# Performance work log

Hardware: AMD Instinct MI355X
Metric: run time of the kernel (lower is better)

Reference implementation:

```python
import jax, jax.numpy as jnp
import numpy as np
import math

B, N, D = 4, 2048, 512
H, DH = 8, 128
INNER = H * DH


def setup_inputs() -> dict:
    key = jax.random.key(0)
    k1, k2, k3, k4 = jax.random.split(key, 4)
    x = jax.random.normal(k1, (B, N, D), dtype=jnp.float32)
    Wg = jax.random.normal(k2, (D, INNER), dtype=jnp.float32) * (1.0 / math.sqrt(D))
    Wout = jax.random.normal(k3, (INNER, D), dtype=jnp.float32) * (1.0 / math.sqrt(INNER))
    sigma = jax.random.uniform(k4, (1, H, 1, 1), dtype=jnp.float32, minval=0.5, maxval=2.5)
    return {"x": x, "Wg": Wg, "Wout": Wout, "sigma": sigma}


def reference(x, Wg, Wout, sigma):
    b, n, d = x.shape
    h, dh = H, DH
    # value projection: [b,n,d] @ [d, h*dh] -> [b,h,n,dh]
    v = (x @ Wg).reshape(b, n, h, dh).transpose(0, 2, 1, 3)
    # fixed Gaussian positional mask, shared across batch: build once per head
    pos = jnp.arange(1, n + 1, dtype=jnp.float32)
    diffs = jnp.abs(pos[:, None] - pos[None, :])  # [n, n]
    sig = sigma.reshape(h, 1, 1)  # [h,1,1]
    inv_norm = 1.0 / (jnp.sqrt(2.0 * jnp.float32(math.pi)) * sig)
    gauss = inv_norm * jnp.exp(-(diffs[None] ** 2) / (2.0 * sig ** 2))  # [h,n,n]
    corr = gauss / gauss.sum(-1, keepdims=True)  # row-normalized [h,n,n]
    # attention: broadcast mask over batch
    attn = jnp.einsum('hnm,bhmd->bhnd', corr, v)
    out = attn.transpose(0, 2, 1, 3).reshape(b, n, h * dh)
    return out @ Wout  # dropout p=0.0 -> identity
```

## Files before the change

kernel.cpp:

```cpp
#include <hip/hip_runtime.h>
#include <hip/hip_bf16.h>
#include <math.h>

#define B_ 4
#define N_ 2048
#define D_ 512
#define H_ 8
#define DH_ 128
#define INNER_ 1024
#define W_ 32
#define M_ (B_ * N_)

typedef __attribute__((ext_vector_type(8))) short short8;
typedef __attribute__((ext_vector_type(4))) float floatx4;

typedef const __attribute__((address_space(1))) char* gcp;
typedef __attribute__((address_space(3))) char* lcp;

__device__ __forceinline__ float bf16hi_to_f(unsigned u) {
    union { unsigned u; float f; } c; c.u = u; return c.f;
}

template <typename OutT>
__global__ __launch_bounds__(256, 4) void gemm_bf16_dbuf(
    const __hip_bfloat16* __restrict__ A, const __hip_bfloat16* __restrict__ Bt,
    OutT* __restrict__ C, int M, int N, int K)
{
    __shared__ char smem[32768];

    const int tid  = threadIdx.x;
    const int lane = tid & 63;
    const int w    = tid >> 6;
    const int wm   = w >> 1;
    const int wn   = w & 1;
    const int bm   = blockIdx.y;
    const int bn   = blockIdx.x;

    const int kh = lane >> 4;
    const int ml = lane & 15;

    floatx4 acc[2][2];
    #pragma unroll
    for (int i = 0; i < 2; ++i)
        #pragma unroll
        for (int j = 0; j < 2; ++j) acc[i][j] = (floatx4){0.f, 0.f, 0.f, 0.f};

    const char* Ab = (const char*)(A + (size_t)(bm * 64) * K);
    const char* Bb = (const char*)(Bt + (size_t)(bn * 64) * K);
    const size_t rowstride = (size_t)K * 2;

    auto issue = [&](int buf, int k0) {
        #pragma unroll
        for (int it = 0; it < 2; ++it) {
            int o = it * 4096 + tid * 16;
            int r = o >> 7;
            int s = (o >> 4) & 7;
            int c = s ^ (r & 7);
            size_t goff = (size_t)r * rowstride + (size_t)k0 * 2 + c * 16;
            __builtin_amdgcn_global_load_lds((gcp)(Ab + goff),
                (lcp)(smem + buf * 16384 + o), 16, 0, 0);
            __builtin_amdgcn_global_load_lds((gcp)(Bb + goff),
                (lcp)(smem + buf * 16384 + 8192 + o), 16, 0, 0);
        }
    };

    auto consume = [&](int buf) {
        const short* As = (const short*)(smem + buf * 16384);
        const short* Bs = (const short*)(smem + buf * 16384 + 8192);
        short8 af[2][2], bf[2][2];
        #pragma unroll
        for (int t = 0; t < 2; ++t) {
            int ra = wm * 32 + t * 16 + ml;
            int rb = wn * 32 + t * 16 + ml;
            #pragma unroll
            for (int kk = 0; kk < 2; ++kk) {
                int ch = kk * 4 + kh;
                af[t][kk] = *(const short8*)(As + ra * 64 + ((ch ^ (ra & 7)) * 8));
                bf[t][kk] = *(const short8*)(Bs + rb * 64 + ((ch ^ (rb & 7)) * 8));
            }
        }
        #pragma unroll
        for (int kk = 0; kk < 2; ++kk)
            #pragma unroll
            for (int i = 0; i < 2; ++i)
                #pragma unroll
                for (int j = 0; j < 2; ++j)
                    acc[i][j] = __builtin_amdgcn_mfma_f32_16x16x32_bf16(
                        af[i][kk], bf[j][kk], acc[i][j], 0, 0, 0);
    };

    const int nk = K >> 6;
    issue(0, 0);
    for (int kt = 0; kt < nk; kt += 2) {
        __syncthreads();
        if (kt + 1 < nk) issue(1, (kt + 1) << 6);
        consume(0);
        __syncthreads();
        if (kt + 2 < nk) issue(0, (kt + 2) << 6);
        consume(1);
    }
    __syncthreads();

    float* Cs = (float*)smem;
    const int rq = lane >> 4;
    const int cl = lane & 15;
    #pragma unroll
    for (int i = 0; i < 2; ++i)
        #pragma unroll
        for (int j = 0; j < 2; ++j)
            #pragma unroll
            for (int r = 0; r < 4; ++r)
                Cs[(wm * 32 + i * 16 + rq * 4 + r) * 64 + wn * 32 + j * 16 + cl] = acc[i][j][r];
    __syncthreads();

    if constexpr (sizeof(OutT) == 2) {
        #pragma unroll
        for (int p = 0; p < 2; ++p) {
            int idx = p * 256 + tid;
            int rr = idx >> 3;
            int cc = (idx & 7) * 8;
            const float* src = Cs + rr * 64 + cc;
            __hip_bfloat16 o[8];
            #pragma unroll
            for (int e = 0; e < 8; ++e) o[e] = __float2bfloat16(src[e]);
            *(short8*)((__hip_bfloat16*)C + (size_t)(bm * 64 + rr) * N + bn * 64 + cc) = *(short8*)o;
        }
    } else {
        #pragma unroll
        for (int p = 0; p < 4; ++p) {
            int idx = p * 256 + tid;
            int rr = idx >> 4;
            int cc = (idx & 15) * 4;
            float4 vv = *(const float4*)(Cs + rr * 64 + cc);
            *(float4*)((float*)C + (size_t)(bm * 64 + rr) * N + bn * 64 + cc) = vv;
        }
    }
}

__device__ __forceinline__ void transpose32(
    const float* __restrict__ src, __hip_bfloat16* __restrict__ dst,
    int R, int Cn, int rt, int ct, int tid)
{
    __shared__ float t[32][33];
    int c0 = ct * 32, r0 = rt * 32;
    int lx = tid & 31, ly = tid >> 5;
    #pragma unroll
    for (int i = 0; i < 32; i += 8)
        t[ly + i][lx] = src[(size_t)(r0 + ly + i) * Cn + c0 + lx];
    __syncthreads();
    #pragma unroll
    for (int i = 0; i < 32; i += 8)
        dst[(size_t)(c0 + ly + i) * R + r0 + lx] = __float2bfloat16(t[lx][ly + i]);
}

__global__ __launch_bounds__(256) void prep(
    const float* __restrict__ x, const float* __restrict__ Wg,
    const float* __restrict__ Wout, __hip_bfloat16* __restrict__ x_bf,
    __hip_bfloat16* __restrict__ Wg_t, __hip_bfloat16* __restrict__ Wout_t)
{
    const int bid = blockIdx.x;
    const int tid = threadIdx.x;
    if (bid < 2048) {
        int i = bid * 256 + tid;
        const float4* s = (const float4*)x + (size_t)i * 2;
        float4 a = s[0], b = s[1];
        __hip_bfloat16 o[8] = {
            __float2bfloat16(a.x), __float2bfloat16(a.y), __float2bfloat16(a.z), __float2bfloat16(a.w),
            __float2bfloat16(b.x), __float2bfloat16(b.y), __float2bfloat16(b.z), __float2bfloat16(b.w)};
        *(short8*)(x_bf + (size_t)i * 8) = *(short8*)o;
    } else if (bid < 2560) {
        int id2 = bid - 2048;
        transpose32(Wg, Wg_t, D_, INNER_, id2 >> 5, id2 & 31, tid);
    } else {
        int id2 = bid - 2560;
        transpose32(Wout, Wout_t, INNER_, D_, id2 >> 4, id2 & 15, tid);
    }
}

#define TNA 64
#define ROWSB (TNA + 2 * W_)
#define CHB 64

struct bf16x4s { __hip_bfloat16 a, b, c, d; };

__global__ __launch_bounds__(256) void banded_attn3(
    const __hip_bfloat16* __restrict__ v, const float* __restrict__ sigma,
    __hip_bfloat16* __restrict__ attn)
{
    __shared__ __hip_bfloat16 vs[ROWSB][CHB];
    __shared__ float wtab[2 * W_ + 1];
    __shared__ float winv[TNA];

    const int tid = threadIdx.x;
    const int n0  = blockIdx.x * TNA;
    const int h   = blockIdx.y >> 1;
    const int ch0 = (blockIdx.y & 1) * CHB;
    const int b   = blockIdx.z;

    const __hip_bfloat16* vbase = v + (size_t)b * N_ * INNER_ + h * DH_ + ch0;
    #pragma unroll
    for (int it = 0; it < 4; ++it) {
        int idx = tid + it * 256;
        int r = idx >> 3;
        int g = idx & 7;
        int m = n0 - W_ + r;
        int4 val = make_int4(0, 0, 0, 0);
        if (m >= 0 && m < N_) val = *(const int4*)(vbase + (size_t)m * INNER_ + g * 8);
        *(int4*)&vs[r][g * 8] = val;
    }
    if (tid <= 2 * W_) {
        float sig = sigma[h];
        float d = (float)(tid - W_);
        wtab[tid] = __expf(-d * d / (2.0f * sig * sig));
    }
    __syncthreads();

    if (tid < TNA) {
        int n = n0 + tid;
        float ws = 0.f;
        #pragma unroll
        for (int j = 0; j <= 2 * W_; ++j) {
            int m = n - W_ + j;
            ws += (m >= 0 && m < N_) ? wtab[j] : 0.f;
        }
        winv[tid] = 1.0f / ws;
    }
    __syncthreads();

    const int cg = tid & 15;
    const int rg = tid >> 4;

    float4 acc[4];
    #pragma unroll
    for (int r = 0; r < 4; ++r) acc[r] = make_float4(0.f, 0.f, 0.f, 0.f);
    float wreg[4] = {0.f, 0.f, 0.f, 0.f};

    const unsigned* vrow0 = (const unsigned*)&vs[rg * 4][cg * 4];

    #pragma unroll 4
    for (int l = 0; l < 2 * W_ + 4; ++l) {
        wreg[l & 3] = (l <= 2 * W_) ? wtab[l] : 0.f;
        const unsigned* p = vrow0 + (size_t)l * (CHB / 2);
        unsigned r0 = p[0], r1 = p[1];
        float4 vv;
        vv.x = bf16hi_to_f(r0 << 16);
        vv.y = bf16hi_to_f(r0 & 0xffff0000u);
        vv.z = bf16hi_to_f(r1 << 16);
        vv.w = bf16hi_to_f(r1 & 0xffff0000u);
        #pragma unroll
        for (int r = 0; r < 4; ++r) {
            float wgt = wreg[(l - r) & 3];
            acc[r].x += wgt * vv.x; acc[r].y += wgt * vv.y;
            acc[r].z += wgt * vv.z; acc[r].w += wgt * vv.w;
        }
    }

    #pragma unroll
    for (int r = 0; r < 4; ++r) {
        int nl = rg * 4 + r;
        float s = winv[nl];
        bf16x4s o = { __float2bfloat16(acc[r].x * s), __float2bfloat16(acc[r].y * s),
                      __float2bfloat16(acc[r].z * s), __float2bfloat16(acc[r].w * s) };
        *(bf16x4s*)(attn + ((size_t)b * N_ + n0 + nl) * INNER_ + h * DH_ + ch0 + cg * 4) = o;
    }
}

extern "C" void kernel_launch(void* const* d_in, const int* in_sizes, int n_in,
                              void* d_out, int out_size, void* d_ws, size_t ws_size,
                              hipStream_t stream) {
    const float* x     = (const float*)d_in[0];
    const float* Wg    = (const float*)d_in[1];
    const float* Wout  = (const float*)d_in[2];
    const float* sigma = (const float*)d_in[3];
    float* out = (float*)d_out;

    char* ws = (char*)d_ws;
    __hip_bfloat16* x_bf   = (__hip_bfloat16*)ws;
    __hip_bfloat16* Wg_t   = (__hip_bfloat16*)(ws + (((size_t)8)  << 20));
    __hip_bfloat16* Wout_t = (__hip_bfloat16*)(ws + (((size_t)9)  << 20));
    __hip_bfloat16* v_bf   = (__hip_bfloat16*)(ws + (((size_t)10) << 20));
    __hip_bfloat16* attn   = (__hip_bfloat16*)(ws + (((size_t)26) << 20));

    prep<<<dim3(3072), dim3(256), 0, stream>>>(x, Wg, Wout, x_bf, Wg_t, Wout_t);

    gemm_bf16_dbuf<__hip_bfloat16><<<dim3(INNER_ / 64, M_ / 64), dim3(256), 0, stream>>>(
        x_bf, Wg_t, v_bf, M_, INNER_, D_);

    banded_attn3<<<dim3(N_ / TNA, H_ * 2, B_), dim3(256), 0, stream>>>(v_bf, sigma, attn);

    gemm_bf16_dbuf<float><<<dim3(D_ / 64, M_ / 64), dim3(256), 0, stream>>>(
        attn, Wout_t, out, M_, D_, INNER_);
}
```

Baseline: 136.2 us.

## Fuse value projection GEMM with banded Gaussian blur in one kernel

Replaces the separate value-projection GEMM and banded attention kernels with one kernel. Each block computes a 128-row slab of v (64 output rows plus a 32-row halo on each side) for one head with MFMA, stages it in LDS as bf16, and then applies the normalized Gaussian band directly. This removes the global write and re-read of the full v tensor and one launch. The cost is recomputing the halo rows, which roughly doubles the projection FLOPs. The K loop is single-buffered. The column permutation that the LDS packing introduces is undone by permuting the K axis of the transposed Wout.

After: 130.2 us. -4.4%, faster.

```diff
diff --git a/kernel.cpp b/kernel.cpp
--- a/kernel.cpp
+++ b/kernel.cpp
@@ -19,6 +19,162 @@
 
 __device__ __forceinline__ float bf16hi_to_f(unsigned u) {
     union { unsigned u; float f; } c; c.u = u; return c.f;
+}
+__device__ __forceinline__ unsigned f_to_bf16bits(float f) {
+    union { float f; unsigned u; } c; c.f = f;
+    return (c.u + 0x7fffu + ((c.u >> 16) & 1u)) >> 16;
+}
+
+struct bf16x4s { __hip_bfloat16 a, b, c, d; };
+
+__global__ __launch_bounds__(256, 4) void g1_blur(
+    const __hip_bfloat16* __restrict__ x_bf,
+    const __hip_bfloat16* __restrict__ Wg_t,
+    const float* __restrict__ sigma,
+    __hip_bfloat16* __restrict__ attn)
+{
+    __shared__ char smem[33824];
+    __hip_bfloat16* Asm = (__hip_bfloat16*)smem;
+    __hip_bfloat16* Bsm = (__hip_bfloat16*)(smem + 16384);
+
+    const int tid  = threadIdx.x;
+    const int lane = tid & 63;
+    const int w    = tid >> 6;
+    const int wm   = w >> 1;
+    const int wn   = w & 1;
+    const int quad = lane >> 4;
+    const int cl   = lane & 15;
+    const int bm   = blockIdx.x;
+    const int h    = blockIdx.y;
+    const int n0   = bm * 64;
+    const int nb0  = n0 & (N_ - 1);
+
+    floatx4 acc[4][4];
+    #pragma unroll
+    for (int i = 0; i < 4; ++i)
+        #pragma unroll
+        for (int j = 0; j < 4; ++j) acc[i][j] = (floatx4){0.f, 0.f, 0.f, 0.f};
+
+    const char* Ab = (const char*)x_bf;
+    const char* Bb = (const char*)(Wg_t + (size_t)(h * DH_) * D_);
+
+    for (int k0 = 0; k0 < D_; k0 += 64) {
+        #pragma unroll
+        for (int it = 0; it < 4; ++it) {
+            int o = it * 4096 + tid * 16;
+            int r = o >> 7;
+            int s = (o >> 4) & 7;
+            int c = s ^ (r & 7);
+            int gr = n0 - W_ + r;
+            gr = gr < 0 ? 0 : (gr > M_ - 1 ? M_ - 1 : gr);
+            __builtin_amdgcn_global_load_lds(
+                (gcp)(Ab + (size_t)gr * 1024 + k0 * 2 + c * 16), (lcp)(smem + o), 16, 0, 0);
+            __builtin_amdgcn_global_load_lds(
+                (gcp)(Bb + (size_t)r * 1024 + k0 * 2 + c * 16), (lcp)(smem + 16384 + o), 16, 0, 0);
+        }
+        __syncthreads();
+
+        const short* As = (const short*)Asm;
+        const short* Bs = (const short*)Bsm;
+        #pragma unroll
+        for (int kk = 0; kk < 2; ++kk) {
+            short8 af[4], bf[4];
+            int ch = kk * 4 + quad;
+            #pragma unroll
+            for (int t = 0; t < 4; ++t) {
+                int ra = wm * 64 + t * 16 + cl;
+                int rb = wn * 64 + t * 16 + cl;
+                af[t] = *(const short8*)(As + ra * 64 + ((ch ^ (ra & 7)) * 8));
+                bf[t] = *(const short8*)(Bs + rb * 64 + ((ch ^ (rb & 7)) * 8));
+            }
+            #pragma unroll
+            for (int i = 0; i < 4; ++i)
+                #pragma unroll
+                for (int j = 0; j < 4; ++j)
+                    acc[i][j] = __builtin_amdgcn_mfma_f32_16x16x32_bf16(
+                        af[i], bf[j], acc[i][j], 0, 0, 0);
+        }
+        __syncthreads();
+    }
+
+    unsigned short* vsp = (unsigned short*)smem;
+    float* wtab = (float*)(smem + 33280);
+    float* winv = (float*)(smem + 33280 + 272);
+
+    #pragma unroll
+    for (int i = 0; i < 4; ++i) {
+        #pragma unroll
+        for (int jp = 0; jp < 2; ++jp) {
+            #pragma unroll
+            for (int rr = 0; rr < 4; ++rr) {
+                int srow = wm * 64 + i * 16 + quad * 4 + rr;
+                int vb = nb0 - W_ + srow;
+                unsigned u = 0u;
+                if (vb >= 0 && vb < N_) {
+                    unsigned lo = f_to_bf16bits(acc[i][jp * 2][rr]);
+                    unsigned hi = f_to_bf16bits(acc[i][jp * 2 + 1][rr]);
+                    u = lo | (hi << 16);
+                }
+                int scol = wn * 64 + jp * 32 + cl * 2;
+                *(unsigned*)(vsp + srow * 130 + scol) = u;
+            }
+        }
+    }
+    if (tid <= 2 * W_) {
+        float sig = sigma[h];
+        float d = (float)(tid - W_);
+        wtab[tid] = __expf(-d * d / (2.0f * sig * sig));
+    }
+    __syncthreads();
+
+    if (tid < 64) {
+        int nbl = nb0 + tid;
+        float ws = 0.f;
+        #pragma unroll
+        for (int j = 0; j <= 2 * W_; ++j) {
+            int m = nbl - W_ + j;
+            ws += (m >= 0 && m < N_) ? wtab[j] : 0.f;
+        }
+        winv[tid] = 1.0f / ws;
+    }
+
+    const int cg = tid & 31;
+    const int rg = tid >> 5;
+
+    float4 bacc[8];
+    #pragma unroll
+    for (int r = 0; r < 8; ++r) bacc[r] = make_float4(0.f, 0.f, 0.f, 0.f);
+    float wreg[8] = {0.f, 0.f, 0.f, 0.f, 0.f, 0.f, 0.f, 0.f};
+
+    const unsigned* vrow0 = (const unsigned*)(vsp + rg * 8 * 130 + cg * 4);
+
+    #pragma unroll 8
+    for (int l = 0; l < 2 * W_ + 8; ++l) {
+        wreg[l & 7] = (l <= 2 * W_) ? wtab[l] : 0.f;
+        const unsigned* p = vrow0 + (size_t)l * 65;
+        unsigned r0 = p[0], r1 = p[1];
+        float4 vv;
+        vv.x = bf16hi_to_f(r0 << 16);
+        vv.y = bf16hi_to_f(r0 & 0xffff0000u);
+        vv.z = bf16hi_to_f(r1 << 16);
+        vv.w = bf16hi_to_f(r1 & 0xffff0000u);
+        #pragma unroll
+        for (int r = 0; r < 8; ++r) {
+            float wgt = wreg[(l - r) & 7];
+            bacc[r].x += wgt * vv.x; bacc[r].y += wgt * vv.y;
+            bacc[r].z += wgt * vv.z; bacc[r].w += wgt * vv.w;
+        }
+    }
+    __syncthreads();
+
+    #pragma unroll
+    for (int r = 0; r < 8; ++r) {
+        int o = rg * 8 + r;
+        float s = winv[o];
+        bf16x4s ov = { __float2bfloat16(bacc[r].x * s), __float2bfloat16(bacc[r].y * s),
+                       __float2bfloat16(bacc[r].z * s), __float2bfloat16(bacc[r].w * s) };
+        *(bf16x4s*)(attn + (size_t)(n0 + o) * INNER_ + h * DH_ + cg * 4) = ov;
+    }
 }
 
 template <typename OutT>
@@ -63,7 +219,6 @@
                 (lcp)(smem + buf * 16384 + 8192 + o), 16, 0, 0);
         }
     };
-
     auto consume = [&](int buf) {
         const short* As = (const short*)(smem + buf * 16384);
         const short* Bs = (const short*)(smem + buf * 16384 + 8192);
@@ -137,7 +292,8 @@
     }
 }
 
-__device__ __forceinline__ void transpose32(
+template <bool PERM>
+__device__ __forceinline__ void transpose32p(
     const float* __restrict__ src, __hip_bfloat16* __restrict__ dst,
     int R, int Cn, int rt, int ct, int tid)
 {
@@ -148,9 +304,10 @@
     for (int i = 0; i < 32; i += 8)
         t[ly + i][lx] = src[(size_t)(r0 + ly + i) * Cn + c0 + lx];
     __syncthreads();
+    int colx = PERM ? (r0 + ((lx & 15) * 2 | (lx >> 4))) : (r0 + lx);
     #pragma unroll
     for (int i = 0; i < 32; i += 8)
-        dst[(size_t)(c0 + ly + i) * R + r0 + lx] = __float2bfloat16(t[lx][ly + i]);
+        dst[(size_t)(c0 + ly + i) * R + colx] = __float2bfloat16(t[lx][ly + i]);
 }
 
 __global__ __launch_bounds__(256) void prep(
@@ -170,98 +327,10 @@
         *(short8*)(x_bf + (size_t)i * 8) = *(short8*)o;
     } else if (bid < 2560) {
         int id2 = bid - 2048;
-        transpose32(Wg, Wg_t, D_, INNER_, id2 >> 5, id2 & 31, tid);
+        transpose32p<false>(Wg, Wg_t, D_, INNER_, id2 >> 5, id2 & 31, tid);
     } else {
         int id2 = bid - 2560;
-        transpose32(Wout, Wout_t, INNER_, D_, id2 >> 4, id2 & 15, tid);
-    }
-}
-
-#define TNA 64
-#define ROWSB (TNA + 2 * W_)
-#define CHB 64
-
-struct bf16x4s { __hip_bfloat16 a, b, c, d; };
-
-__global__ __launch_bounds__(256) void banded_attn3(
-    const __hip_bfloat16* __restrict__ v, const float* __restrict__ sigma,
-    __hip_bfloat16* __restrict__ attn)
-{
-    __shared__ __hip_bfloat16 vs[ROWSB][CHB];
-    __shared__ float wtab[2 * W_ + 1];
-    __shared__ float winv[TNA];
-
-    const int tid = threadIdx.x;
-    const int n0  = blockIdx.x * TNA;
-    const int h   = blockIdx.y >> 1;
-    const int ch0 = (blockIdx.y & 1) * CHB;
-    const int b   = blockIdx.z;
-
-    const __hip_bfloat16* vbase = v + (size_t)b * N_ * INNER_ + h * DH_ + ch0;
-    #pragma unroll
-    for (int it = 0; it < 4; ++it) {
-        int idx = tid + it * 256;
-        int r = idx >> 3;
-        int g = idx & 7;
-        int m = n0 - W_ + r;
-        int4 val = make_int4(0, 0, 0, 0);
-        if (m >= 0 && m < N_) val = *(const int4*)(vbase + (size_t)m * INNER_ + g * 8);
-        *(int4*)&vs[r][g * 8] = val;
-    }
-    if (tid <= 2 * W_) {
-        float sig = sigma[h];
-        float d = (float)(tid - W_);
-        wtab[tid] = __expf(-d * d / (2.0f * sig * sig));
-    }
-    __syncthreads();
-
-    if (tid < TNA) {
-        int n = n0 + tid;
-        float ws = 0.f;
-        #pragma unroll
-        for (int j = 0; j <= 2 * W_; ++j) {
-            int m = n - W_ + j;
-            ws += (m >= 0 && m < N_) ? wtab[j] : 0.f;
-        }
-        winv[tid] = 1.0f / ws;
-    }
-    __syncthreads();
-
-    const int cg = tid & 15;
-    const int rg = tid >> 4;
-
-    float4 acc[4];
-    #pragma unroll
-    for (int r = 0; r < 4; ++r) acc[r] = make_float4(0.f, 0.f, 0.f, 0.f);
-    float wreg[4] = {0.f, 0.f, 0.f, 0.f};
-
-    const unsigned* vrow0 = (const unsigned*)&vs[rg * 4][cg * 4];
-
-    #pragma unroll 4
-    for (int l = 0; l < 2 * W_ + 4; ++l) {
-        wreg[l & 3] = (l <= 2 * W_) ? wtab[l] : 0.f;
-        const unsigned* p = vrow0 + (size_t)l * (CHB / 2);
-        unsigned r0 = p[0], r1 = p[1];
-        float4 vv;
-        vv.x = bf16hi_to_f(r0 << 16);
-        vv.y = bf16hi_to_f(r0 & 0xffff0000u);
-        vv.z = bf16hi_to_f(r1 << 16);
-        vv.w = bf16hi_to_f(r1 & 0xffff0000u);
-        #pragma unroll
-        for (int r = 0; r < 4; ++r) {
-            float wgt = wreg[(l - r) & 3];
-            acc[r].x += wgt * vv.x; acc[r].y += wgt * vv.y;
-            acc[r].z += wgt * vv.z; acc[r].w += wgt * vv.w;
-        }
-    }
-
-    #pragma unroll
-    for (int r = 0; r < 4; ++r) {
-        int nl = rg * 4 + r;
-        float s = winv[nl];
-        bf16x4s o = { __float2bfloat16(acc[r].x * s), __float2bfloat16(acc[r].y * s),
-                      __float2bfloat16(acc[r].z * s), __float2bfloat16(acc[r].w * s) };
-        *(bf16x4s*)(attn + ((size_t)b * N_ + n0 + nl) * INNER_ + h * DH_ + ch0 + cg * 4) = o;
+        transpose32p<true>(Wout, Wout_t, INNER_, D_, id2 >> 4, id2 & 15, tid);
     }
 }
 
@@ -278,15 +347,11 @@
     __hip_bfloat16* x_bf   = (__hip_bfloat16*)ws;
     __hip_bfloat16* Wg_t   = (__hip_bfloat16*)(ws + (((size_t)8)  << 20));
     __hip_bfloat16* Wout_t = (__hip_bfloat16*)(ws + (((size_t)9)  << 20));
-    __hip_bfloat16* v_bf   = (__hip_bfloat16*)(ws + (((size_t)10) << 20));
-    __hip_bfloat16* attn   = (__hip_bfloat16*)(ws + (((size_t)26) << 20));
+    __hip_bfloat16* attn   = (__hip_bfloat16*)(ws + (((size_t)10) << 20));
 
     prep<<<dim3(3072), dim3(256), 0, stream>>>(x, Wg, Wout, x_bf, Wg_t, Wout_t);
 
-    gemm_bf16_dbuf<__hip_bfloat16><<<dim3(INNER_ / 64, M_ / 64), dim3(256), 0, stream>>>(
-        x_bf, Wg_t, v_bf, M_, INNER_, D_);
-
-    banded_attn3<<<dim3(N_ / TNA, H_ * 2, B_), dim3(256), 0, stream>>>(v_bf, sigma, attn);
+    g1_blur<<<dim3(M_ / 64, H_), dim3(256), 0, stream>>>(x_bf, Wg_t, sigma, attn);
 
     gemm_bf16_dbuf<float><<<dim3(D_ / 64, M_ / 64), dim3(256), 0, stream>>>(
         attn, Wout_t, out, M_, D_, INNER_);
```
